# Performance work log

Measured on AMD Instinct MI355X. Metric: run time of the kernel, lower is better.

The kernel has to match this reference:

```python
import jax, jax.numpy as jnp
import numpy as np

N = 100000   # nodes
E = 1600000  # edges
IN = 128     # in_channels
H = 96       # hidden
G = 512      # graphs in batch


def setup_inputs() -> dict:
    key = jax.random.key(0)
    ks = jax.random.split(key, 11)
    x = jax.random.normal(ks[0], (N, IN), jnp.float32)
    edge_index = jax.random.randint(ks[1], (2, E), 0, N)
    batch = jnp.sort(jax.random.randint(ks[2], (N,), 0, G))
    def lin(k, fan_in, fan_out):
        lim = 1.0 / np.sqrt(fan_in)
        kw, kb = jax.random.split(k)
        W = jax.random.uniform(kw, (fan_in, fan_out), jnp.float32, -lim, lim)
        b = jax.random.uniform(kb, (fan_out,), jnp.float32, -lim, lim)
        return W, b
    W1, b1 = lin(ks[3], IN, H)
    W2, b2 = lin(ks[4], H, H)
    Wn, bn = lin(ks[5], 2 * H, 1)
    Wg, bg = lin(ks[6], 4 * H, 1)
    return dict(x=x, edge_index=edge_index, batch=batch,
                W1=W1, b1=b1, W2=W2, b2=b2, Wn=Wn, bn=bn, Wg=Wg, bg=bg)


def reference(x, edge_index, batch, W1, b1, W2, b2, Wn, bn, Wg, bg):
    # --- GCN normalization with self-loops: D^-1/2 (A+I) D^-1/2 ---
    loops = jnp.arange(N)
    src = jnp.concatenate([edge_index[0], loops])  # [E+N]
    dst = jnp.concatenate([edge_index[1], loops])
    deg = jax.ops.segment_sum(jnp.ones_like(dst, jnp.float32), dst, num_segments=N)
    dis = jnp.where(deg > 0, jax.lax.rsqrt(jnp.maximum(deg, 1.0)), 0.0)
    norm = dis[src] * dis[dst]  # [E+N]

    def gcn_conv(h, W, b):
        hw = h @ W                                # transform first (smaller msgs)
        msg = hw[src] * norm[:, None]             # gather + scale  [E+N, H]
        return jax.ops.segment_sum(msg, dst, num_segments=N) + b

    h1 = jax.nn.relu(gcn_conv(x, W1, b1))         # dropout: eval no-op
    h2 = jax.nn.relu(gcn_conv(h1, W2, b2))
    h = jnp.concatenate([h1, h2], axis=1)         # [N, 2H]

    node_logits = (h @ Wn + bn).reshape(-1)       # [N]

    cnt = jax.ops.segment_sum(jnp.ones((N,), jnp.float32), batch, num_segments=G)
    meanp = jax.ops.segment_sum(h, batch, num_segments=G) / jnp.maximum(cnt, 1.0)[:, None]
    maxp = jax.ops.segment_max(h, batch, num_segments=G)
    maxp = jnp.where(cnt[:, None] > 0, maxp, 0.0)
    pooled = jnp.concatenate([meanp, maxp], axis=1)  # [G, 4H]

    graph_logits = (pooled @ Wg + bg).reshape(-1)    # [G]
    return graph_logits, node_logits
```

## Files before the change

### kernel.cpp

```cpp
#include <hip/hip_runtime.h>
#include <hip/hip_fp16.h>

#define NN 100000
#define NE 1600000
#define INC 128
#define HID 96
#define NG 512

#define GEMM1_BLOCKS 1563
#define G2_BLOCKS 1563

#define BK_SHIFT 9
#define BK_SIZE 512
#define NBK 196
#define A_EPB 4096
#define A_BLOCKS 391

typedef _Float16 half8 __attribute__((ext_vector_type(8)));
typedef float f32x4 __attribute__((ext_vector_type(4)));

__global__ __launch_bounds__(256) void k_pack_a1(const int* __restrict__ dst,
                                                 int* __restrict__ histAB,
                                                 const float* __restrict__ W1,
                                                 const float* __restrict__ W2,
                                                 __half* __restrict__ W1frag,
                                                 __half* __restrict__ W2frag) {
    const int tid = threadIdx.x;
    if (blockIdx.x < A_BLOCKS) {
        __shared__ int cnt[NBK];
        int ab = blockIdx.x;
        for (int i = tid; i < NBK; i += 256) cnt[i] = 0;
        __syncthreads();
        int e0 = ab * A_EPB;
#pragma unroll 4
        for (int q = 0; q < A_EPB / 256; ++q) {
            int e = e0 + q * 256 + tid;
            if (e < NE) atomicAdd(&cnt[dst[e] >> BK_SHIFT], 1);
        }
        __syncthreads();
        for (int i = tid; i < NBK; i += 256) histAB[ab * NBK + i] = cnt[i];
        return;
    }
    int p = (blockIdx.x - A_BLOCKS) * 256 + tid;
    if (p < 1536) {
        int kc = p / 384;
        int rem = p - kc * 384;
        int ct = rem >> 6;
        int l = rem & 63;
#pragma unroll
        for (int i = 0; i < 8; ++i) {
            int k = kc * 32 + ((l >> 4) << 3) + i;
            int c = ct * 16 + (l & 15);
            W1frag[p * 8 + i] = __float2half(W1[k * HID + c]);
        }
    } else {
        int q = p - 1536;
        if (q >= 1152) return;
        int kc = q / 384;
        int rem = q - kc * 384;
        int ct = rem >> 6;
        int l = rem & 63;
#pragma unroll
        for (int i = 0; i < 8; ++i) {
            int k = kc * 32 + ((l >> 4) << 3) + i;
            int c = ct * 16 + (l & 15);
            W2frag[q * 8 + i] = __float2half(W2[k * HID + c]);
        }
    }
}

__global__ __launch_bounds__(256) void k_scanS(int* __restrict__ histAB, int* __restrict__ boff) {
    __shared__ int tot[256];
    int t = threadIdx.x;
    int run = 0;
    if (t < NBK) {
        for (int blk = 0; blk < A_BLOCKS; ++blk) {
            int idx = blk * NBK + t;
            int v = histAB[idx];
            histAB[idx] = run;
            run += v;
        }
    }
    tot[t] = (t < NBK) ? run : 0;
    __syncthreads();
    for (int ofs = 1; ofs < 256; ofs <<= 1) {
        int v = (t >= ofs) ? tot[t - ofs] : 0;
        __syncthreads();
        tot[t] += v;
        __syncthreads();
    }
    if (t == 0) boff[0] = 0;
    if (t < NBK) boff[t + 1] = tot[t];
}

__global__ __launch_bounds__(256) void k_gemm1_a3(
        const float* __restrict__ X, const __half* __restrict__ W1frag,
        __half* __restrict__ Yh,
        const int* __restrict__ src, const int* __restrict__ dst,
        const int* __restrict__ boff, const int* __restrict__ histAB,
        unsigned* __restrict__ tmp) {
    __shared__ __half w1s[12288];
    const int tid = threadIdx.x;

    if (blockIdx.x < A_BLOCKS) {
        int* base = (int*)w1s;
        int* lcnt = base + NBK;
        int ab = blockIdx.x;
        for (int i = tid; i < NBK; i += 256) {
            base[i] = boff[i] + histAB[ab * NBK + i];
            lcnt[i] = 0;
        }
        __syncthreads();
        int e0 = ab * A_EPB;
#pragma unroll 4
        for (int q = 0; q < A_EPB / 256; ++q) {
            int e = e0 + q * 256 + tid;
            if (e < NE) {
                int d = dst[e];
                int bk = d >> BK_SHIFT;
                int lp = atomicAdd(&lcnt[bk], 1);
                tmp[base[bk] + lp] = (unsigned)src[e] | ((unsigned)(d & (BK_SIZE - 1)) << 17);
            }
        }
        return;
    }

    {
        half8* d8 = (half8*)w1s;
        const half8* s8 = (const half8*)W1frag;
        for (int i = tid; i < 1536; i += 256) d8[i] = s8[i];
    }
    __syncthreads();
    const int w = tid >> 6;
    const int l = tid & 63;
    const int row0 = (blockIdx.x - A_BLOCKS) * 64 + w * 16;
    int arow = row0 + (l & 15);
    if (arow >= NN) arow = NN - 1;
    f32x4 acc[6] = {};
#pragma unroll
    for (int kc = 0; kc < 4; ++kc) {
        const float* xp = &X[(size_t)arow * INC + kc * 32 + ((l >> 4) << 3)];
        float4 xa = *(const float4*)xp;
        float4 xb = *(const float4*)(xp + 4);
        half8 a;
        a[0] = (_Float16)xa.x; a[1] = (_Float16)xa.y;
        a[2] = (_Float16)xa.z; a[3] = (_Float16)xa.w;
        a[4] = (_Float16)xb.x; a[5] = (_Float16)xb.y;
        a[6] = (_Float16)xb.z; a[7] = (_Float16)xb.w;
#pragma unroll
        for (int ct = 0; ct < 6; ++ct) {
            half8 b = *(const half8*)&w1s[((kc * 6 + ct) * 64 + l) * 8];
            acc[ct] = __builtin_amdgcn_mfma_f32_16x16x32_f16(a, b, acc[ct], 0, 0, 0);
        }
    }
    const int orow = row0 + ((l >> 4) << 2);
    const int col = l & 15;
#pragma unroll
    for (int ct = 0; ct < 6; ++ct)
#pragma unroll
        for (int i = 0; i < 4; ++i) {
            int r = orow + i;
            if (r < NN) Yh[(size_t)r * HID + ct * 16 + col] = __float2half(acc[ct][i]);
        }
}

__global__ __launch_bounds__(256) void k_B1(const unsigned* __restrict__ tmp,
                                            const int* __restrict__ boff,
                                            int* __restrict__ off, float* __restrict__ dis) {
    __shared__ int cnt[BK_SIZE];
    __shared__ int psum[256];
    const int t = threadIdx.x;
    const int b = blockIdx.x;
    const int nb = b << BK_SHIFT;
    const int rbeg = boff[b], rend = boff[b + 1];
    cnt[t] = 0; cnt[t + 256] = 0;
    __syncthreads();
    for (int e = rbeg + t; e < rend; e += 256) {
        unsigned u = tmp[e];
        atomicAdd(&cnt[u >> 17], 1);
    }
    __syncthreads();
    int c0 = cnt[2 * t], c1 = cnt[2 * t + 1];
    int pairSum = c0 + c1;
    psum[t] = pairSum;
    __syncthreads();
    for (int ofs = 1; ofs < 256; ofs <<= 1) {
        int v = (t >= ofs) ? psum[t - ofs] : 0;
        __syncthreads();
        psum[t] += v;
        __syncthreads();
    }
    int pairExcl = psum[t] - pairSum;
    int node0 = nb + 2 * t, node1 = node0 + 1;
    if (node0 < NN) {
        off[node0] = rbeg + pairExcl;
        dis[node0] = rsqrtf((float)(c0 + 1));
    }
    if (node1 < NN) {
        off[node1] = rbeg + pairExcl + c0;
        dis[node1] = rsqrtf((float)(c1 + 1));
    }
    if (b == NBK - 1 && t == 0) off[NN] = rend;
}

__global__ __launch_bounds__(256) void k_B2(const unsigned* __restrict__ tmp,
                                            const int* __restrict__ boff,
                                            const int* __restrict__ off,
                                            const float* __restrict__ dis,
                                            int2* __restrict__ ssrcw) {
    __shared__ int cnt[BK_SIZE];
    const int tid = threadIdx.x;
    const int b = blockIdx.x;
    const int nb = b << BK_SHIFT;
    const int rbeg = boff[b], rend = boff[b + 1];
    cnt[tid] = 0; cnt[tid + 256] = 0;
    __syncthreads();
    for (int e = rbeg + tid; e < rend; e += 256) {
        unsigned u = tmp[e];
        int s = (int)(u & 0x1FFFFu);
        int dl = (int)(u >> 17);
        int d = nb + dl;
        int pos = off[d] + atomicAdd(&cnt[dl], 1);
        float w = dis[s] * dis[d];
        ssrcw[pos] = make_int2(s, __float_as_int(w));
    }
}

__global__ __launch_bounds__(256) void k_gemm2(const __half* __restrict__ Xh,
                                               const __half* __restrict__ W2frag,
                                               __half* __restrict__ Yh) {
    __shared__ __half w2s[9216];
    const int tid = threadIdx.x;
    {
        half8* d8 = (half8*)w2s;
        const half8* s8 = (const half8*)W2frag;
        for (int i = tid; i < 1152; i += 256) d8[i] = s8[i];
    }
    __syncthreads();
    const int w = tid >> 6;
    const int l = tid & 63;
    const int row0 = blockIdx.x * 64 + w * 16;
    int arow = row0 + (l & 15);
    if (arow >= NN) arow = NN - 1;
    f32x4 acc[6] = {};
#pragma unroll
    for (int kc = 0; kc < 3; ++kc) {
        half8 a = *(const half8*)&Xh[(size_t)arow * HID + kc * 32 + ((l >> 4) << 3)];
#pragma unroll
        for (int ct = 0; ct < 6; ++ct) {
            half8 b = *(const half8*)&w2s[((kc * 6 + ct) * 64 + l) * 8];
            acc[ct] = __builtin_amdgcn_mfma_f32_16x16x32_f16(a, b, acc[ct], 0, 0, 0);
        }
    }
    const int orow = row0 + ((l >> 4) << 2);
    const int col = l & 15;
#pragma unroll
    for (int ct = 0; ct < 6; ++ct)
#pragma unroll
        for (int i = 0; i < 4; ++i) {
            int r = orow + i;
            if (r < NN) Yh[(size_t)r * HID + ct * 16 + col] = __float2half(acc[ct][i]);
        }
}

template <int B>
__device__ __forceinline__ void agg_batch(const __half* __restrict__ Ah,
                                          const int2* __restrict__ ssrcw, int j, int t,
                                          float& a0x, float& a0y, float& a1x, float& a1y,
                                          float& a2x, float& a2y) {
    long ed[B];
#pragma unroll
    for (int q = 0; q < B; ++q)
        ed[q] = __builtin_nontemporal_load((const long*)&ssrcw[j + q]);
    float w[B];
    const __half2* ap[B];
#pragma unroll
    for (int q = 0; q < B; ++q) {
        int s = (int)(unsigned)(ed[q] & 0xFFFFFFFFL);
        w[q] = __int_as_float((int)(ed[q] >> 32));
        ap[q] = (const __half2*)(Ah + (size_t)s * HID);
    }
    __half2 g0[B], g1[B], g2[B];
#pragma unroll
    for (int q = 0; q < B; ++q) {
        g0[q] = ap[q][t];
        g1[q] = ap[q][t + 16];
        g2[q] = ap[q][t + 32];
    }
#pragma unroll
    for (int q = 0; q < B; ++q) {
        float2 f0 = __half22float2(g0[q]);
        float2 f1 = __half22float2(g1[q]);
        float2 f2 = __half22float2(g2[q]);
        a0x += f0.x * w[q]; a0y += f0.y * w[q];
        a1x += f1.x * w[q]; a1y += f1.y * w[q];
        a2x += f2.x * w[q]; a2y += f2.y * w[q];
    }
}

template <int PHASE>
__global__ __launch_bounds__(256) void k_agg(const __half* __restrict__ Ah,
                                             const int2* __restrict__ ssrcw,
                                             const int* __restrict__ off,
                                             const float* __restrict__ dis,
                                             const float* __restrict__ bias,
                                             const float* __restrict__ Wn,
                                             const float* __restrict__ bn,
                                             __half* __restrict__ outh,
                                             float* __restrict__ nodeOut) {
    int gid = blockIdx.x * blockDim.x + threadIdx.x;
    int d = gid >> 4;
    int t = gid & 15;
    if (d >= NN) return;
    const int beg = off[d], end = off[d + 1];
    const float dd = dis[d];
    const __half2* ad2 = (const __half2*)(Ah + (size_t)d * HID);
    float2 s0 = __half22float2(ad2[t]);
    float2 s1 = __half22float2(ad2[t + 16]);
    float2 s2 = __half22float2(ad2[t + 32]);
    const float dd2 = dd * dd;
    float a0x = s0.x * dd2, a0y = s0.y * dd2;
    float a1x = s1.x * dd2, a1y = s1.y * dd2;
    float a2x = s2.x * dd2, a2y = s2.y * dd2;
    int j = beg;
    for (; j + 11 < end; j += 12)
        agg_batch<12>(Ah, ssrcw, j, t, a0x, a0y, a1x, a1y, a2x, a2y);
    for (; j + 3 < end; j += 4)
        agg_batch<4>(Ah, ssrcw, j, t, a0x, a0y, a1x, a1y, a2x, a2y);
    for (; j < end; ++j) {
        int2 e0 = ssrcw[j];
        float w0 = __int_as_float(e0.y);
        const __half2* a0 = (const __half2*)(Ah + (size_t)e0.x * HID);
        float2 f0 = __half22float2(a0[t]);
        float2 f1 = __half22float2(a0[t + 16]);
        float2 f2 = __half22float2(a0[t + 32]);
        a0x += f0.x * w0; a0y += f0.y * w0;
        a1x += f1.x * w0; a1y += f1.y * w0;
        a2x += f2.x * w0; a2y += f2.y * w0;
    }
    const float2* b2p = (const float2*)bias;
    float2 b0 = b2p[t], b1 = b2p[t + 16], b2 = b2p[t + 32];
    float h0x = fmaxf(a0x + b0.x, 0.f), h0y = fmaxf(a0y + b0.y, 0.f);
    float h1x = fmaxf(a1x + b1.x, 0.f), h1y = fmaxf(a1y + b1.y, 0.f);
    float h2x = fmaxf(a2x + b2.x, 0.f), h2y = fmaxf(a2y + b2.y, 0.f);
    __half2* o2 = (__half2*)(outh + (size_t)d * HID);
    o2[t]      = __floats2half2_rn(h0x, h0y);
    o2[t + 16] = __floats2half2_rn(h1x, h1y);
    o2[t + 32] = __floats2half2_rn(h2x, h2y);

    const int woff = (PHASE == 1) ? 0 : 96;
    const float2* wn2 = (const float2*)(Wn + woff);
    float2 w0v = wn2[t], w1v = wn2[t + 16], w2v = wn2[t + 32];
    float partial = h0x * w0v.x + h0y * w0v.y + h1x * w1v.x + h1y * w1v.y +
                    h2x * w2v.x + h2y * w2v.y;
#pragma unroll
    for (int m = 8; m; m >>= 1) partial += __shfl_down(partial, m, 16);
    if (t == 0) {
        if (PHASE == 1) nodeOut[d] = partial + bn[0];
        else            nodeOut[d] += partial;
    }
}

__global__ __launch_bounds__(768) void k_pool(const __half* __restrict__ h1,
                                              const __half* __restrict__ h2,
                                              const int* __restrict__ batch,
                                              const float* __restrict__ Wg,
                                              const float* __restrict__ bg,
                                              float* __restrict__ out) {
    int g = blockIdx.x;
    int tid = threadIdx.x;
    int way = tid / 192;
    int f = tid - way * 192;

    int lo = 0, hi = NN;
    while (lo < hi) { int mid = (lo + hi) >> 1; if (batch[mid] < g) lo = mid + 1; else hi = mid; }
    int start = lo;
    hi = NN;
    while (lo < hi) { int mid = (lo + hi) >> 1; if (batch[mid] < g + 1) lo = mid + 1; else hi = mid; }
    int end = lo;

    const __half* hsrc = (f < HID) ? h1 : h2;
    int ff = (f < HID) ? f : f - HID;
    float sum = 0.f, mx = 0.f;
    int n = start + way;
    for (; n + 4 < end; n += 8) {
        float v0 = __half2float(hsrc[(size_t)n * HID + ff]);
        float v1 = __half2float(hsrc[(size_t)(n + 4) * HID + ff]);
        sum += v0 + v1;
        mx = fmaxf(mx, fmaxf(v0, v1));
    }
    if (n < end) {
        float v0 = __half2float(hsrc[(size_t)n * HID + ff]);
        sum += v0;
        mx = fmaxf(mx, v0);
    }
    __shared__ float rsum[4][192];
    __shared__ float rmax[4][192];
    rsum[way][f] = sum;
    rmax[way][f] = mx;
    __syncthreads();
    if (way == 0) {
        sum = rsum[0][f] + rsum[1][f] + rsum[2][f] + rsum[3][f];
        mx = fmaxf(fmaxf(rmax[0][f], rmax[1][f]), fmaxf(rmax[2][f], rmax[3][f]));
        float cnt = (float)(end - start);
        float mean = sum / fmaxf(cnt, 1.0f);
        rsum[0][f] = mean * Wg[f] + mx * Wg[192 + f];
    }
    __syncthreads();
    if (tid < 64) {
        float acc = rsum[0][tid] + rsum[0][tid + 64] + rsum[0][tid + 128];
#pragma unroll
        for (int m = 32; m; m >>= 1) acc += __shfl_down(acc, m, 64);
        if (tid == 0) out[g] = acc + bg[0];
    }
}

extern "C" void kernel_launch(void* const* d_in, const int* in_sizes, int n_in,
                              void* d_out, int out_size, void* d_ws, size_t ws_size,
                              hipStream_t stream) {
    const float* x    = (const float*)d_in[0];
    const int*   ei   = (const int*)d_in[1];
    const int*   srcp = ei;
    const int*   dstp = ei + NE;
    const int*   batch = (const int*)d_in[2];
    const float* W1 = (const float*)d_in[3];
    const float* b1 = (const float*)d_in[4];
    const float* W2 = (const float*)d_in[5];
    const float* b2 = (const float*)d_in[6];
    const float* Wn = (const float*)d_in[7];
    const float* bn = (const float*)d_in[8];
    const float* Wg = (const float*)d_in[9];
    const float* bg = (const float*)d_in[10];
    float* out = (float*)d_out;

    char* p = (char*)d_ws;
    auto alloc = [&](size_t bytes) {
        char* r = p;
        p += (bytes + 255) & ~(size_t)255;
        return (void*)r;
    };
    float*    dis    = (float*)alloc(NN * 4);
    int*      off    = (int*)alloc((NN + 1) * 4);
    int*      boff   = (int*)alloc((NBK + 1) * 4);
    int*      histAB = (int*)alloc((size_t)A_BLOCKS * NBK * 4);
    unsigned* tmp    = (unsigned*)alloc((size_t)NE * 4);
    int2*     ssrcw  = (int2*)alloc((size_t)NE * 8);
    __half*   Ah     = (__half*)alloc((size_t)NN * HID * 2);
    __half*   H1h    = (__half*)alloc((size_t)NN * HID * 2);
    __half*   H2h    = (__half*)alloc((size_t)NN * HID * 2);
    __half*   W1frag = (__half*)alloc(12288 * 2);
    __half*   W2frag = (__half*)alloc(9216 * 2);

    const int TPB = 256;

    k_pack_a1<<<A_BLOCKS + 11, TPB, 0, stream>>>(dstp, histAB, W1, W2, W1frag, W2frag);
    k_scanS<<<1, 256, 0, stream>>>(histAB, boff);
    k_gemm1_a3<<<A_BLOCKS + GEMM1_BLOCKS, 256, 0, stream>>>(
        x, W1frag, Ah, srcp, dstp, boff, histAB, tmp);
    k_B1<<<NBK, 256, 0, stream>>>(tmp, boff, off, dis);
    k_B2<<<NBK, 256, 0, stream>>>(tmp, boff, off, dis, ssrcw);

    const int aggThreads = NN * 16;
    float* nodeOut = out + NG;

    k_agg<1><<<(aggThreads + TPB - 1) / TPB, TPB, 0, stream>>>(Ah, ssrcw, off, dis, b1, Wn, bn, H1h, nodeOut);

    k_gemm2<<<G2_BLOCKS, 256, 0, stream>>>(H1h, W2frag, Ah);

    k_agg<2><<<(aggThreads + TPB - 1) / TPB, TPB, 0, stream>>>(Ah, ssrcw, off, dis, b2, Wn, bn, H2h, nodeOut);

    k_pool<<<NG, 768, 0, stream>>>(H1h, H2h, batch, Wg, bg, out);
}
```

Measured before the change: 244.0 us.

## Merge CSR build kernels and compute edge weights on the fly in aggregation

Fuses the count/scan kernel and the scatter kernel into one, using a shared-memory cursor array so the second pass over the bucket no longer reads off[] from global memory. The CSR edge array now stores only source indices (4 bytes instead of 8) and the aggregation kernels recompute each edge weight as dis[src]*dis[dst] with an extra gather. This halves edge-stream traffic and removes one launch, at the cost of a random dis[] lookup per edge in both aggregation passes.

```diff
diff --git a/kernel.cpp b/kernel.cpp
--- a/kernel.cpp
+++ b/kernel.cpp
@@ -164,11 +164,13 @@
         }
 }
 
-__global__ __launch_bounds__(256) void k_B1(const unsigned* __restrict__ tmp,
-                                            const int* __restrict__ boff,
-                                            int* __restrict__ off, float* __restrict__ dis) {
+__global__ __launch_bounds__(256) void k_B(const unsigned* __restrict__ tmp,
+                                           const int* __restrict__ boff,
+                                           int* __restrict__ off, float* __restrict__ dis,
+                                           int* __restrict__ ssrc) {
     __shared__ int cnt[BK_SIZE];
     __shared__ int psum[256];
+    __shared__ int cur[BK_SIZE];
     const int t = threadIdx.x;
     const int b = blockIdx.x;
     const int nb = b << BK_SHIFT;
@@ -191,6 +193,8 @@
         __syncthreads();
     }
     int pairExcl = psum[t] - pairSum;
+    cur[2 * t] = pairExcl;
+    cur[2 * t + 1] = pairExcl + c0;
     int node0 = nb + 2 * t, node1 = node0 + 1;
     if (node0 < NN) {
         off[node0] = rbeg + pairExcl;
@@ -201,28 +205,12 @@
         dis[node1] = rsqrtf((float)(c1 + 1));
     }
     if (b == NBK - 1 && t == 0) off[NN] = rend;
-}
-
-__global__ __launch_bounds__(256) void k_B2(const unsigned* __restrict__ tmp,
-                                            const int* __restrict__ boff,
-                                            const int* __restrict__ off,
-                                            const float* __restrict__ dis,
-                                            int2* __restrict__ ssrcw) {
-    __shared__ int cnt[BK_SIZE];
-    const int tid = threadIdx.x;
-    const int b = blockIdx.x;
-    const int nb = b << BK_SHIFT;
-    const int rbeg = boff[b], rend = boff[b + 1];
-    cnt[tid] = 0; cnt[tid + 256] = 0;
-    __syncthreads();
-    for (int e = rbeg + tid; e < rend; e += 256) {
+    __syncthreads();
+    for (int e = rbeg + t; e < rend; e += 256) {
         unsigned u = tmp[e];
-        int s = (int)(u & 0x1FFFFu);
         int dl = (int)(u >> 17);
-        int d = nb + dl;
-        int pos = off[d] + atomicAdd(&cnt[dl], 1);
-        float w = dis[s] * dis[d];
-        ssrcw[pos] = make_int2(s, __float_as_int(w));
+        int pos = rbeg + atomicAdd(&cur[dl], 1);
+        ssrc[pos] = (int)(u & 0x1FFFFu);
     }
 }
 
@@ -265,20 +253,20 @@
 
 template <int B>
 __device__ __forceinline__ void agg_batch(const __half* __restrict__ Ah,
-                                          const int2* __restrict__ ssrcw, int j, int t,
+                                          const int* __restrict__ ssrc,
+                                          const float* __restrict__ dis, float dd,
+                                          int j, int t,
                                           float& a0x, float& a0y, float& a1x, float& a1y,
                                           float& a2x, float& a2y) {
-    long ed[B];
-#pragma unroll
-    for (int q = 0; q < B; ++q)
-        ed[q] = __builtin_nontemporal_load((const long*)&ssrcw[j + q]);
+    int s[B];
+#pragma unroll
+    for (int q = 0; q < B; ++q) s[q] = ssrc[j + q];
     float w[B];
     const __half2* ap[B];
 #pragma unroll
     for (int q = 0; q < B; ++q) {
-        int s = (int)(unsigned)(ed[q] & 0xFFFFFFFFL);
-        w[q] = __int_as_float((int)(ed[q] >> 32));
-        ap[q] = (const __half2*)(Ah + (size_t)s * HID);
+        w[q] = dis[s[q]] * dd;
+        ap[q] = (const __half2*)(Ah + (size_t)s[q] * HID);
     }
     __half2 g0[B], g1[B], g2[B];
 #pragma unroll
@@ -300,7 +288,7 @@
 
 template <int PHASE>
 __global__ __launch_bounds__(256) void k_agg(const __half* __restrict__ Ah,
-                                             const int2* __restrict__ ssrcw,
+                                             const int* __restrict__ ssrc,
                                              const int* __restrict__ off,
                                              const float* __restrict__ dis,
                                              const float* __restrict__ bias,
@@ -324,13 +312,13 @@
     float a2x = s2.x * dd2, a2y = s2.y * dd2;
     int j = beg;
     for (; j + 11 < end; j += 12)
-        agg_batch<12>(Ah, ssrcw, j, t, a0x, a0y, a1x, a1y, a2x, a2y);
+        agg_batch<12>(Ah, ssrc, dis, dd, j, t, a0x, a0y, a1x, a1y, a2x, a2y);
     for (; j + 3 < end; j += 4)
-        agg_batch<4>(Ah, ssrcw, j, t, a0x, a0y, a1x, a1y, a2x, a2y);
+        agg_batch<4>(Ah, ssrc, dis, dd, j, t, a0x, a0y, a1x, a1y, a2x, a2y);
     for (; j < end; ++j) {
-        int2 e0 = ssrcw[j];
-        float w0 = __int_as_float(e0.y);
-        const __half2* a0 = (const __half2*)(Ah + (size_t)e0.x * HID);
+        int s = ssrc[j];
+        float w0 = dis[s] * dd;
+        const __half2* a0 = (const __half2*)(Ah + (size_t)s * HID);
         float2 f0 = __half22float2(a0[t]);
         float2 f1 = __half22float2(a0[t + 16]);
         float2 f2 = __half22float2(a0[t + 32]);
@@ -444,7 +432,7 @@
     int*      boff   = (int*)alloc((NBK + 1) * 4);
     int*      histAB = (int*)alloc((size_t)A_BLOCKS * NBK * 4);
     unsigned* tmp    = (unsigned*)alloc((size_t)NE * 4);
-    int2*     ssrcw  = (int2*)alloc((size_t)NE * 8);
+    int*      ssrc   = (int*)alloc((size_t)NE * 4);
     __half*   Ah     = (__half*)alloc((size_t)NN * HID * 2);
     __half*   H1h    = (__half*)alloc((size_t)NN * HID * 2);
     __half*   H2h    = (__half*)alloc((size_t)NN * HID * 2);
@@ -457,17 +445,16 @@
     k_scanS<<<1, 256, 0, stream>>>(histAB, boff);
     k_gemm1_a3<<<A_BLOCKS + GEMM1_BLOCKS, 256, 0, stream>>>(
         x, W1frag, Ah, srcp, dstp, boff, histAB, tmp);
-    k_B1<<<NBK, 256, 0, stream>>>(tmp, boff, off, dis);
-    k_B2<<<NBK, 256, 0, stream>>>(tmp, boff, off, dis, ssrcw);
+    k_B<<<NBK, 256, 0, stream>>>(tmp, boff, off, dis, ssrc);
 
     const int aggThreads = NN * 16;
     float* nodeOut = out + NG;
 
-    k_agg<1><<<(aggThreads + TPB - 1) / TPB, TPB, 0, stream>>>(Ah, ssrcw, off, dis, b1, Wn, bn, H1h, nodeOut);
+    k_agg<1><<<(aggThreads + TPB - 1) / TPB, TPB, 0, stream>>>(Ah, ssrc, off, dis, b1, Wn, bn, H1h, nodeOut);
 
     k_gemm2<<<G2_BLOCKS, 256, 0, stream>>>(H1h, W2frag, Ah);
 
-    k_agg<2><<<(aggThreads + TPB - 1) / TPB, TPB, 0, stream>>>(Ah, ssrcw, off, dis, b2, Wn, bn, H2h, nodeOut);
+    k_agg<2><<<(aggThreads + TPB - 1) / TPB, TPB, 0, stream>>>(Ah, ssrc, off, dis, b2, Wn, bn, H2h, nodeOut);
 
     k_pool<<<NG, 768, 0, stream>>>(H1h, H2h, batch, Wg, bg, out);
 }
```

Measured after the change: 241.8 us. No clear change (-0.9%).
